# Performance work log

Measured on AMD Instinct MI355X. Metric: run time of the kernel, lower is better.

Reference implementation:

```python
import jax, jax.numpy as jnp
import numpy as np

BATCH, GROUPS, ARITY, OUT_DIM = 1024, 512, 4, 64


def _high_order_act(X, params):
    # X: [B, G, K]; params: [G, 2**K, D]
    A_ind = jnp.argsort(X, axis=2)                                   # [B,G,K] int
    A_sort = jnp.take_along_axis(X, A_ind, axis=2)                   # sorted values
    # barycentric-style coefficients: smallest value, then successive gaps
    coef = jnp.concatenate(
        [A_sort[:, :, :1], A_sort[:, :, 1:] - A_sort[:, :, :-1]], axis=2
    )                                                                 # [B,G,K]
    # reversed cumulative sum of 2**A_ind -> vertex index into 2**K table
    pow2 = jnp.left_shift(jnp.int32(1), A_ind.astype(jnp.int32))      # [B,G,K]
    idx = jnp.flip(jnp.cumsum(jnp.flip(pow2, axis=2), axis=2), axis=2)  # [B,G,K]
    G = params.shape[0]
    g_idx = jnp.arange(G)[None, :, None]                              # [1,G,1]
    pg = params[g_idx, idx]                                           # [B,G,K,D] gather
    return jnp.einsum('bgk,bgkd->bgd', coef, pg)                      # [B,G,D]


def setup_inputs() -> dict:
    key = jax.random.key(0)
    k1, k2 = jax.random.split(key)
    X = jax.random.normal(k1, (BATCH, GROUPS, ARITY), dtype=jnp.float32)
    params = jax.random.normal(k2, (GROUPS, 2 ** ARITY, OUT_DIM), dtype=jnp.float32)
    return {"X": X, "params": params}


def reference(X, params):
    return _high_order_act(X, params)
```

## Files before the change

### kernel.cpp

```cpp
#include <hip/hip_runtime.h>

#define BATCH   1024
#define GROUPS  512
#define OUT_DIM 64
#define G_TILE  4
#define B_TILE  32

typedef float f32x4 __attribute__((ext_vector_type(4)));

__global__ __launch_bounds__(256) void hoact_kernel(
    const float4* __restrict__ X4,
    const float4* __restrict__ P4,
    float4*       __restrict__ O4)
{
    __shared__ float tbl[G_TILE * 16 * 64];

    const int gtile  = blockIdx.x & 127;
    const int bchunk = blockIdx.x >> 7;
    const int g0     = gtile * G_TILE;
    const int b0     = bchunk * B_TILE;
    const int tid    = threadIdx.x;

#pragma unroll
    for (int k = 0; k < 4; ++k) {
        const int q = tid + k * 256;
        *(f32x4*)&tbl[q * 4] = *(const f32x4*)&P4[g0 * 256 + q];
    }

    const int w        = tid >> 6;
    const int gl       = (tid >> 4) & 3;
    const int c4       = tid & 15;
    const int lane64   = tid & 63;
    const int lds_base = gl * 1024;

    float4 xv[8];
#pragma unroll
    for (int p = 0; p < 8; ++p) {
        const int b = b0 + p * 4 + w;
        xv[p] = X4[b * GROUPS + g0 + gl];
    }

    __syncthreads();

#pragma unroll
    for (int p = 0; p < 8; ++p) {
        const int b = b0 + p * 4 + w;
        const float4 x = xv[p];

        float v0 = __uint_as_float((__float_as_uint(x.x) & ~3u) | 0u);
        float v1 = __uint_as_float((__float_as_uint(x.y) & ~3u) | 1u);
        float v2 = __uint_as_float((__float_as_uint(x.z) & ~3u) | 2u);
        float v3 = __uint_as_float((__float_as_uint(x.w) & ~3u) | 3u);

#define CSWAP(a, b_)                                 \
        {                                            \
            const float lo = fminf((a), (b_));       \
            const float hi = fmaxf((a), (b_));       \
            (a) = lo; (b_) = hi;                     \
        }
        CSWAP(v0, v1);
        CSWAP(v2, v3);
        CSWAP(v0, v2);
        CSWAP(v1, v3);
        CSWAP(v1, v2);
#undef CSWAP

        const int i1 = __float_as_uint(v1) & 3;
        const int i2 = __float_as_uint(v2) & 3;
        const int i3 = __float_as_uint(v3) & 3;

        const float c0 = v0;
        const float c1 = v1 - v0;
        const float c2 = v2 - v1;
        const float c3 = v3 - v2;

        const int e3 = 1 << i3;
        const int e2 = e3 + (1 << i2);
        const int e1 = e2 + (1 << i1);

        const f32x4 p0 = *(const f32x4*)&tbl[lds_base + 15 * 64 + c4 * 4];
        const f32x4 p1 = *(const f32x4*)&tbl[lds_base + e1 * 64 + c4 * 4];
        const f32x4 p2 = *(const f32x4*)&tbl[lds_base + e2 * 64 + c4 * 4];
        const f32x4 p3 = *(const f32x4*)&tbl[lds_base + e3 * 64 + c4 * 4];

        f32x4 o;
        o.x = c0 * p0.x + c1 * p1.x + c2 * p2.x + c3 * p3.x;
        o.y = c0 * p0.y + c1 * p1.y + c2 * p2.y + c3 * p3.y;
        o.z = c0 * p0.z + c1 * p1.z + c2 * p2.z + c3 * p3.z;
        o.w = c0 * p0.w + c1 * p1.w + c2 * p2.w + c3 * p3.w;

        const int o_idx = b * (GROUPS * 16) + gtile * 64 + lane64;
        __builtin_nontemporal_store(o, (f32x4*)&O4[o_idx]);
    }
}

extern "C" void kernel_launch(void* const* d_in, const int* in_sizes, int n_in,
                              void* d_out, int out_size, void* d_ws, size_t ws_size,
                              hipStream_t stream) {
    const float4* X4 = (const float4*)d_in[0];
    const float4* P4 = (const float4*)d_in[1];
    float4*       O4 = (float4*)d_out;

    const int grid = (GROUPS / G_TILE) * (BATCH / B_TILE);
    hipLaunchKernelGGL(hoact_kernel, dim3(grid), dim3(256), 0, stream,
                       X4, P4, O4);
}
```

Measured before the change: 153.7 us.

## Drop LDS param staging; gather params directly from global memory per batch row

Removes the shared-memory table and the block barrier. Each block now handles half of one batch row's groups and gathers the four parameter rows straight from global memory, relying on L2/L1 caching of the 2 MB parameter table. This avoids reloading the parameter tile into LDS for every block, but the data-dependent gathers now go to the cache hierarchy instead of LDS and may see higher latency or lower hit rates.

```diff
diff --git a/kernel.cpp b/kernel.cpp
--- a/kernel.cpp
+++ b/kernel.cpp
@@ -2,9 +2,6 @@
 
 #define BATCH   1024
 #define GROUPS  512
-#define OUT_DIM 64
-#define G_TILE  4
-#define B_TILE  32
 
 typedef float f32x4 __attribute__((ext_vector_type(4)));
 
@@ -13,84 +10,76 @@
     const float4* __restrict__ P4,
     float4*       __restrict__ O4)
 {
-    __shared__ float tbl[G_TILE * 16 * 64];
+    const int tid = threadIdx.x;
+    const int b   = blockIdx.x >> 1;
+    const int h   = blockIdx.x & 1;
+    const int w   = tid >> 6;
+    const int gl  = (tid >> 4) & 3;
+    const int c4  = tid & 15;
 
-    const int gtile  = blockIdx.x & 127;
-    const int bchunk = blockIdx.x >> 7;
-    const int g0     = gtile * G_TILE;
-    const int b0     = bchunk * B_TILE;
-    const int tid    = threadIdx.x;
+    const int  gw0  = h * 256 + w * 64;
+    const long xoff = (long)b * GROUPS;
+    const long ooff = (long)b * (GROUPS * 16);
 
 #pragma unroll
-    for (int k = 0; k < 4; ++k) {
-        const int q = tid + k * 256;
-        *(f32x4*)&tbl[q * 4] = *(const f32x4*)&P4[g0 * 256 + q];
-    }
-
-    const int w        = tid >> 6;
-    const int gl       = (tid >> 4) & 3;
-    const int c4       = tid & 15;
-    const int lane64   = tid & 63;
-    const int lds_base = gl * 1024;
-
-    float4 xv[8];
+    for (int half = 0; half < 2; ++half) {
+        float4 xv[8];
 #pragma unroll
-    for (int p = 0; p < 8; ++p) {
-        const int b = b0 + p * 4 + w;
-        xv[p] = X4[b * GROUPS + g0 + gl];
-    }
-
-    __syncthreads();
+        for (int j = 0; j < 8; ++j) {
+            const int g = gw0 + (half * 8 + j) * 4 + gl;
+            xv[j] = X4[xoff + g];
+        }
 
 #pragma unroll
-    for (int p = 0; p < 8; ++p) {
-        const int b = b0 + p * 4 + w;
-        const float4 x = xv[p];
+        for (int j = 0; j < 8; ++j) {
+            const int g = gw0 + (half * 8 + j) * 4 + gl;
+            const float4 x = xv[j];
 
-        float v0 = __uint_as_float((__float_as_uint(x.x) & ~3u) | 0u);
-        float v1 = __uint_as_float((__float_as_uint(x.y) & ~3u) | 1u);
-        float v2 = __uint_as_float((__float_as_uint(x.z) & ~3u) | 2u);
-        float v3 = __uint_as_float((__float_as_uint(x.w) & ~3u) | 3u);
+            float v0 = __uint_as_float((__float_as_uint(x.x) & ~3u) | 0u);
+            float v1 = __uint_as_float((__float_as_uint(x.y) & ~3u) | 1u);
+            float v2 = __uint_as_float((__float_as_uint(x.z) & ~3u) | 2u);
+            float v3 = __uint_as_float((__float_as_uint(x.w) & ~3u) | 3u);
 
 #define CSWAP(a, b_)                                 \
-        {                                            \
-            const float lo = fminf((a), (b_));       \
-            const float hi = fmaxf((a), (b_));       \
-            (a) = lo; (b_) = hi;                     \
-        }
-        CSWAP(v0, v1);
-        CSWAP(v2, v3);
-        CSWAP(v0, v2);
-        CSWAP(v1, v3);
-        CSWAP(v1, v2);
+            {                                        \
+                const float lo = fminf((a), (b_));   \
+                const float hi = fmaxf((a), (b_));   \
+                (a) = lo; (b_) = hi;                 \
+            }
+            CSWAP(v0, v1);
+            CSWAP(v2, v3);
+            CSWAP(v0, v2);
+            CSWAP(v1, v3);
+            CSWAP(v1, v2);
 #undef CSWAP
 
-        const int i1 = __float_as_uint(v1) & 3;
-        const int i2 = __float_as_uint(v2) & 3;
-        const int i3 = __float_as_uint(v3) & 3;
+            const int i1 = __float_as_uint(v1) & 3;
+            const int i2 = __float_as_uint(v2) & 3;
+            const int i3 = __float_as_uint(v3) & 3;
 
-        const float c0 = v0;
-        const float c1 = v1 - v0;
-        const float c2 = v2 - v1;
-        const float c3 = v3 - v2;
+            const float c0 = v0;
+            const float c1 = v1 - v0;
+            const float c2 = v2 - v1;
+            const float c3 = v3 - v2;
 
-        const int e3 = 1 << i3;
-        const int e2 = e3 + (1 << i2);
-        const int e1 = e2 + (1 << i1);
+            const int e3 = 1 << i3;
+            const int e2 = e3 + (1 << i2);
+            const int e1 = e2 + (1 << i1);
 
-        const f32x4 p0 = *(const f32x4*)&tbl[lds_base + 15 * 64 + c4 * 4];
-        const f32x4 p1 = *(const f32x4*)&tbl[lds_base + e1 * 64 + c4 * 4];
-        const f32x4 p2 = *(const f32x4*)&tbl[lds_base + e2 * 64 + c4 * 4];
-        const f32x4 p3 = *(const f32x4*)&tbl[lds_base + e3 * 64 + c4 * 4];
+            const int  gbase = g << 8;
+            const f32x4 p0 = *(const f32x4*)&P4[gbase + (15 << 4) + c4];
+            const f32x4 p1 = *(const f32x4*)&P4[gbase + (e1 << 4) + c4];
+            const f32x4 p2 = *(const f32x4*)&P4[gbase + (e2 << 4) + c4];
+            const f32x4 p3 = *(const f32x4*)&P4[gbase + (e3 << 4) + c4];
 
-        f32x4 o;
-        o.x = c0 * p0.x + c1 * p1.x + c2 * p2.x + c3 * p3.x;
-        o.y = c0 * p0.y + c1 * p1.y + c2 * p2.y + c3 * p3.y;
-        o.z = c0 * p0.z + c1 * p1.z + c2 * p2.z + c3 * p3.z;
-        o.w = c0 * p0.w + c1 * p1.w + c2 * p2.w + c3 * p3.w;
+            f32x4 o;
+            o.x = c0 * p0.x + c1 * p1.x + c2 * p2.x + c3 * p3.x;
+            o.y = c0 * p0.y + c1 * p1.y + c2 * p2.y + c3 * p3.y;
+            o.z = c0 * p0.z + c1 * p1.z + c2 * p2.z + c3 * p3.z;
+            o.w = c0 * p0.w + c1 * p1.w + c2 * p2.w + c3 * p3.w;
 
-        const int o_idx = b * (GROUPS * 16) + gtile * 64 + lane64;
-        __builtin_nontemporal_store(o, (f32x4*)&O4[o_idx]);
+            __builtin_nontemporal_store(o, (f32x4*)&O4[ooff + (g << 4) + c4]);
+        }
     }
 }
 
@@ -101,7 +90,7 @@
     const float4* P4 = (const float4*)d_in[1];
     float4*       O4 = (float4*)d_out;
 
-    const int grid = (GROUPS / G_TILE) * (BATCH / B_TILE);
+    const int grid = BATCH * 2;
     hipLaunchKernelGGL(hoact_kernel, dim3(grid), dim3(256), 0, stream,
                        X4, P4, O4);
 }
```

After: 180.2 us. 17.3% more time.
